# Performance work log

Measured on AMD Instinct MI355X. Metric: run time of the kernel, lower is better.

The kernel has to match this reference:

```python
import jax, jax.numpy as jnp
import numpy as np

EPS = 1e-5

def setup_inputs() -> dict:
    key = jax.random.key(0)
    ks = jax.random.split(key, 4)
    B, C, A, T = 32, 1536, 128, 1000  # batch, in_channels, attention_channels, time
    x = jax.random.normal(ks[0], (B, C, T), dtype=jnp.float32)
    # attention MLP: Conv1d(3C -> A, k=1) -> ReLU -> BN(A) -> Conv1d(A -> C, k=1)
    w1 = jax.random.normal(ks[1], (A, 3 * C), dtype=jnp.float32) / np.float32(np.sqrt(3 * C))
    b1 = jnp.zeros((A,), jnp.float32)
    g1 = jnp.ones((A,), jnp.float32)
    be1 = jnp.zeros((A,), jnp.float32)
    rm1 = jnp.zeros((A,), jnp.float32)
    rv1 = jnp.ones((A,), jnp.float32)
    w2 = jax.random.normal(ks[2], (C, A), dtype=jnp.float32) / np.float32(np.sqrt(A))
    b2 = jnp.zeros((C,), jnp.float32)
    # final BatchNorm1d over 2C pooled features
    g2 = jnp.ones((2 * C,), jnp.float32)
    be2 = jnp.zeros((2 * C,), jnp.float32)
    rm2 = jnp.zeros((2 * C,), jnp.float32)
    rv2 = jnp.ones((2 * C,), jnp.float32)
    return {"x": x, "w1": w1, "b1": b1, "g1": g1, "be1": be1, "rm1": rm1, "rv1": rv1,
            "w2": w2, "b2": b2, "g2": g2, "be2": be2, "rm2": rm2, "rv2": rv2}

def reference(x, w1, b1, g1, be1, rm1, rv1, w2, b2, g2, be2, rm2, rv2):
    # x: [B, C, T]
    mean_x = jnp.mean(x, axis=2, keepdims=True)                       # [B,C,1]
    std_x = jnp.sqrt(jnp.var(x, axis=2, ddof=1, keepdims=True) + EPS)  # unbiased var
    cat = jnp.concatenate([x,
                           jnp.broadcast_to(mean_x, x.shape),
                           jnp.broadcast_to(std_x, x.shape)], axis=1)  # [B,3C,T]
    # conv1x1 == channel matmul
    h = jnp.einsum('ac,bct->bat', w1, cat) + b1[None, :, None]         # [B,A,T]
    h = jax.nn.relu(h)
    # BatchNorm1d(A), inference mode with running stats
    h = (h - rm1[None, :, None]) * (g1 / jnp.sqrt(rv1 + EPS))[None, :, None] + be1[None, :, None]
    logits = jnp.einsum('ca,bat->bct', w2, h) + b2[None, :, None]      # [B,C,T]
    attn = jax.nn.softmax(logits, axis=2)
    xs = x * attn
    mu = jnp.sum(xs, axis=2)                                           # [B,C]
    sum_sq = jnp.sum(xs * x, axis=2)                                   # [B,C]
    sigma = jnp.sqrt(jnp.abs(sum_sq - mu ** 2) + EPS)
    pool = jnp.concatenate([mu, sigma], axis=1)                        # [B,2C]
    # final BatchNorm1d(2C), inference mode
    return (pool - rm2) * (g2 / jnp.sqrt(rv2 + EPS)) + be2
```

## Files before the change

### kernel.cpp

```cpp
#include <hip/hip_runtime.h>
#include <hip/hip_bf16.h>

#define BATCH 32
#define CCH   1536
#define ACH   128
#define TLEN  1000
#define TPAD  1024
#define NCB   (CCH / 64)
#define XTB   (TPAD * 64)
#define TSPLIT 4
#define TCHUNK 256
#define TSA   2
#define EPSV  1e-5f
#define NINF  -3.0e38f
#define LOG2E 1.4426950408889634f
#define RTHR  11.5f

typedef __attribute__((ext_vector_type(8))) short bf16x8;
typedef __attribute__((ext_vector_type(4))) float f32x4;

__device__ __forceinline__ unsigned short f2bf(float f) {
    union { float f; unsigned u; } v; v.f = f;
    unsigned r = v.u + 0x7fffu + ((v.u >> 16) & 1u);
    return (unsigned short)(r >> 16);
}
__device__ __forceinline__ float bf2f(unsigned short u) {
    union { unsigned u; float f; } v; v.u = ((unsigned)u) << 16;
    return v.f;
}

__global__ __launch_bounds__(512) void kA(const float* __restrict__ x,
                                          unsigned short* __restrict__ xt,
                                          float* __restrict__ st1,
                                          float* __restrict__ st2) {
    int b = blockIdx.y, cblk = blockIdx.x, ts = blockIdx.z;
    int cb = cblk * 64;
    int tbase = ts * (TPAD / TSA);
    int tid = threadIdx.x;
    int row = tid >> 3, l8 = tid & 7;
    __shared__ float tile[2][64][65];
    __shared__ float red1[8][64], red2[8][64];
    const float* xr = x + ((size_t)(b * CCH + cb + row)) * TLEN + tbase;
    unsigned short* xtp = xt + ((size_t)(b * NCB + cblk)) * XTB + (size_t)tbase * 64;

    float4 rA[2];
    float cs1[8], cs2[8];
    #pragma unroll
    for (int j = 0; j < 8; ++j) { cs1[j] = 0.f; cs2[j] = 0.f; }

    auto loadTile = [&](int it) {
        #pragma unroll
        for (int p = 0; p < 2; ++p) {
            int tf = it * 64 + p * 32 + l8 * 4;
            float4 vv = make_float4(0.f, 0.f, 0.f, 0.f);
            if (tbase + tf < TLEN) vv = *reinterpret_cast<const float4*>(xr + tf);
            rA[p] = vv;
        }
    };
    auto writeTile = [&](int buf) {
        #pragma unroll
        for (int p = 0; p < 2; ++p) {
            int tl = p * 32 + l8 * 4;
            tile[buf][tl + 0][row] = rA[p].x;
            tile[buf][tl + 1][row] = rA[p].y;
            tile[buf][tl + 2][row] = rA[p].z;
            tile[buf][tl + 3][row] = rA[p].w;
        }
    };
    auto readStore = [&](int buf, int it) {
        int tl = tid >> 3;
        int c8 = (tid & 7) * 8;
        float v[8];
        #pragma unroll
        for (int j = 0; j < 8; ++j) {
            v[j] = tile[buf][tl][c8 + j];
            cs1[j] += v[j];
            cs2[j] += v[j] * v[j];
        }
        unsigned o[4];
        #pragma unroll
        for (int j = 0; j < 4; ++j)
            o[j] = (unsigned)f2bf(v[2 * j]) | ((unsigned)f2bf(v[2 * j + 1]) << 16);
        uint4 u; u.x = o[0]; u.y = o[1]; u.z = o[2]; u.w = o[3];
        *reinterpret_cast<uint4*>(xtp + (size_t)(it * 64 + tl) * 64 + c8) = u;
    };

    const int NIT = (TPAD / TSA) / 64;
    loadTile(0);
    writeTile(0);
    loadTile(1);
    __syncthreads();
    for (int it = 0; it < NIT; ++it) {
        int buf = it & 1;
        if (it < NIT - 1) writeTile(buf ^ 1);
        if (it < NIT - 2) loadTile(it + 2);
        readStore(buf, it);
        __syncthreads();
    }

    #pragma unroll
    for (int j = 0; j < 8; ++j) {
        #pragma unroll
        for (int d = 8; d < 64; d <<= 1) {
            cs1[j] += __shfl_xor(cs1[j], d);
            cs2[j] += __shfl_xor(cs2[j], d);
        }
    }
    int wv = tid >> 6, lane = tid & 63;
    if (lane < 8) {
        #pragma unroll
        for (int j = 0; j < 8; ++j) {
            red1[wv][lane * 8 + j] = cs1[j];
            red2[wv][lane * 8 + j] = cs2[j];
        }
    }
    __syncthreads();
    if (tid < 64) {
        float s1 = 0.f, s2 = 0.f;
        #pragma unroll
        for (int w = 0; w < 8; ++w) { s1 += red1[w][tid]; s2 += red2[w][tid]; }
        st1[((size_t)ts * BATCH + b) * CCH + cb + tid] = s1;
        st2[((size_t)ts * BATCH + b) * CCH + cb + tid] = s2;
    }
}

__global__ __launch_bounds__(256) void kA2(const float* __restrict__ x,
                                           float* __restrict__ st1,
                                           float* __restrict__ st2) {
    int b = blockIdx.y, cb = blockIdx.x * 32;
    int tid = threadIdx.x;
    int row = tid >> 3, l8 = tid & 7;
    const float* xr = x + ((size_t)(b * CCH + cb + row)) * TLEN;
    float s1 = 0.f, s2 = 0.f;
    for (int tf = l8 * 4; tf < TLEN; tf += 32) {
        float4 vv = *reinterpret_cast<const float4*>(xr + tf);
        s1 += vv.x + vv.y + vv.z + vv.w;
        s2 += vv.x * vv.x + vv.y * vv.y + vv.z * vv.z + vv.w * vv.w;
    }
    #pragma unroll
    for (int d = 1; d < 8; d <<= 1) { s1 += __shfl_xor(s1, d); s2 += __shfl_xor(s2, d); }
    if (l8 == 0) {
        int idx = b * CCH + cb + row;
        st1[idx] = s1;
        st2[idx] = s2;
        st1[(size_t)BATCH * CCH + idx] = 0.f;
        st2[(size_t)BATCH * CCH + idx] = 0.f;
    }
}

__global__ __launch_bounds__(256) void kBW(const float* __restrict__ w1,
                                           unsigned short* __restrict__ w1x,
                                           const float* __restrict__ w2,
                                           const float* __restrict__ b2,
                                           const float* __restrict__ g1,
                                           const float* __restrict__ be1,
                                           const float* __restrict__ rm1,
                                           const float* __restrict__ rv1,
                                           unsigned short* __restrict__ w2e,
                                           float* __restrict__ b2e) {
    int bx = blockIdx.x;
    const int NB1 = (ACH * CCH) / 256;
    if (bx < NB1) {
        int e = bx * 256 + threadIdx.x;
        int a = e / CCH, c = e - a * CCH;
        w1x[e] = f2bf(w1[(size_t)a * (3 * CCH) + c]);
    } else {
        int c = (bx - NB1) * 4 + (threadIdx.x >> 6);
        int l = threadIdx.x & 63;
        float acc = 0.f;
        #pragma unroll
        for (int p = 0; p < 2; ++p) {
            int a = p * 64 + l;
            float s1 = g1[a] * rsqrtf(rv1[a] + EPSV);
            float w = w2[(size_t)c * ACH + a];
            w2e[(size_t)c * ACH + a] = f2bf(w * s1 * LOG2E);
            acc += w * (be1[a] - s1 * rm1[a]);
        }
        #pragma unroll
        for (int d = 1; d < 64; d <<= 1) acc += __shfl_xor(acc, d);
        if (l == 0) b2e[c] = (b2[c] + acc) * LOG2E;
    }
}

__global__ __launch_bounds__(64) void kB2n(const float* __restrict__ w1,
                                           const float* __restrict__ b1,
                                           const float* __restrict__ st1,
                                           const float* __restrict__ st2,
                                           float* __restrict__ hbias) {
    int a = blockIdx.x, b = blockIdx.y, l = threadIdx.x;
    const float* wr = w1 + (size_t)a * 3 * CCH;
    const float* p1 = st1 + (size_t)b * CCH;
    const float* p2 = st2 + (size_t)b * CCH;
    const size_t half = (size_t)BATCH * CCH;
    float acc = 0.f;
    const float invT = 1.f / (float)TLEN;
    const float invT1 = 1.f / (float)(TLEN - 1);
    for (int k = l; k < CCH; k += 64) {
        float s1 = p1[k] + p1[half + k];
        float s2 = p2[k] + p2[half + k];
        float mean = s1 * invT;
        float var = (s2 - s1 * s1 * invT) * invT1;
        float stdv = sqrtf(var + EPSV);
        acc += wr[CCH + k] * mean + wr[2 * CCH + k] * stdv;
    }
    #pragma unroll
    for (int d = 1; d < 64; d <<= 1) acc += __shfl_xor(acc, d);
    if (l == 0) hbias[b * ACH + a] = acc + b1[a];
}

__global__ __launch_bounds__(512) void kC3(const unsigned short* __restrict__ xt,
                                           const unsigned short* __restrict__ w1x,
                                           const float* __restrict__ hbias,
                                           unsigned short* __restrict__ h) {
    int b = blockIdx.y;
    int t0 = blockIdx.x * 64;
    int tid = threadIdx.x;
    int wv = tid >> 6, l = tid & 63, g = l >> 4, r = l & 15;
    int a0 = (wv & 3) * 32;
    int tw = (wv >> 2) * 32;

    __shared__ uint4 As[2][1024];
    __shared__ uint4 Bs[2][512];

    const unsigned short* bG = xt + (size_t)b * NCB * XTB;

    int qa0 = tid, qa1 = tid + 512, qb = tid;
    int wa0 = qa0 ^ ((qa0 >> 3) & 7), wa1 = qa1 ^ ((qa1 >> 3) & 7), wb = qb ^ ((qb >> 3) & 7);
    int arow0 = qa0 >> 3, arow1 = qa1 >> 3, acol = (qa0 & 7) * 8;
    int brow = qb >> 3, bcol = (qb & 7) * 8;

    As[0][wa0] = *reinterpret_cast<const uint4*>(w1x + (size_t)arow0 * CCH + acol);
    As[0][wa1] = *reinterpret_cast<const uint4*>(w1x + (size_t)arow1 * CCH + acol);
    Bs[0][wb]  = *reinterpret_cast<const uint4*>(bG + (size_t)(t0 + brow) * 64 + bcol);
    __syncthreads();

    f32x4 acc[2][2];
    #pragma unroll
    for (int i = 0; i < 2; ++i)
        #pragma unroll
        for (int j = 0; j < 2; ++j) acc[i][j] = f32x4{0.f, 0.f, 0.f, 0.f};

    for (int ks = 0; ks < CCH / 64; ++ks) {
        int buf = ks & 1;
        uint4 na0, na1, nb;
        if (ks < CCH / 64 - 1) {
            int cofs = (ks + 1) * 64;
            na0 = *reinterpret_cast<const uint4*>(w1x + (size_t)arow0 * CCH + cofs + acol);
            na1 = *reinterpret_cast<const uint4*>(w1x + (size_t)arow1 * CCH + cofs + acol);
            nb  = *reinterpret_cast<const uint4*>(bG + (size_t)(ks + 1) * XTB + (size_t)(t0 + brow) * 64 + bcol);
        }
        bf16x8 Af[2][2], Bf[2][2];
        #pragma unroll
        for (int at = 0; at < 2; ++at) {
            int row = a0 + 16 * at + r;
            #pragma unroll
            for (int kk = 0; kk < 2; ++kk) {
                int ch = (row * 8 + kk * 4 + g) ^ (row & 7);
                Af[at][kk] = *reinterpret_cast<const bf16x8*>(&As[buf][ch]);
            }
        }
        #pragma unroll
        for (int tt = 0; tt < 2; ++tt) {
            int row = tw + 16 * tt + r;
            #pragma unroll
            for (int kk = 0; kk < 2; ++kk) {
                int ch = (row * 8 + kk * 4 + g) ^ (row & 7);
                Bf[tt][kk] = *reinterpret_cast<const bf16x8*>(&Bs[buf][ch]);
            }
        }
        #pragma unroll
        for (int kk = 0; kk < 2; ++kk)
            #pragma unroll
            for (int at = 0; at < 2; ++at)
                #pragma unroll
                for (int tt = 0; tt < 2; ++tt)
                    acc[at][tt] = __builtin_amdgcn_mfma_f32_16x16x32_bf16(Af[at][kk], Bf[tt][kk], acc[at][tt], 0, 0, 0);
        if (ks < CCH / 64 - 1) {
            As[buf ^ 1][wa0] = na0;
            As[buf ^ 1][wa1] = na1;
            Bs[buf ^ 1][wb]  = nb;
        }
        __syncthreads();
    }

    #pragma unroll
    for (int at = 0; at < 2; ++at) {
        f32x4 hb = *reinterpret_cast<const f32x4*>(hbias + b * ACH + a0 + 16 * at + 4 * g);
        #pragma unroll
        for (int tt = 0; tt < 2; ++tt) {
            int t = t0 + tw + 16 * tt + r;
            float v0 = acc[at][tt][0] + hb[0]; v0 = v0 > 0.f ? v0 : 0.f;
            float v1 = acc[at][tt][1] + hb[1]; v1 = v1 > 0.f ? v1 : 0.f;
            float v2 = acc[at][tt][2] + hb[2]; v2 = v2 > 0.f ? v2 : 0.f;
            float v3 = acc[at][tt][3] + hb[3]; v3 = v3 > 0.f ? v3 : 0.f;
            uint2 u;
            u.x = (unsigned)f2bf(v0) | ((unsigned)f2bf(v1) << 16);
            u.y = (unsigned)f2bf(v2) | ((unsigned)f2bf(v3) << 16);
            *reinterpret_cast<uint2*>(h + ((size_t)(b * TPAD + t)) * ACH + a0 + 16 * at + 4 * g) = u;
        }
    }
}

__global__ __launch_bounds__(256) void kC2(const float* __restrict__ x,
                                           const unsigned short* __restrict__ w1x,
                                           const float* __restrict__ hbias,
                                           unsigned short* __restrict__ h) {
    int b = blockIdx.y;
    int t0 = blockIdx.x * 32;
    int tid = threadIdx.x;
    int wv = tid >> 6, l = tid & 63, g = l >> 4, r = l & 15;
    const unsigned short* aptr = w1x + (size_t)(32 * wv + r) * CCH + 8 * g;
    f32x4 acc[2][2];
    #pragma unroll
    for (int i = 0; i < 2; ++i)
        #pragma unroll
        for (int j = 0; j < 2; ++j) acc[i][j] = f32x4{0.f, 0.f, 0.f, 0.f};
    for (int kk = 0; kk < CCH / 32; ++kk) {
        bf16x8 Af[2], Bf[2];
        #pragma unroll
        for (int at = 0; at < 2; ++at)
            Af[at] = *reinterpret_cast<const bf16x8*>(aptr + (size_t)(16 * at) * CCH + 32 * kk);
        #pragma unroll
        for (int tt = 0; tt < 2; ++tt) {
            int t = t0 + 16 * tt + r;
            unsigned short tmp[8];
            #pragma unroll
            for (int j = 0; j < 8; ++j) {
                float xv = 0.f;
                if (t < TLEN) xv = x[((size_t)(b * CCH + 32 * kk + 8 * g + j)) * TLEN + t];
                tmp[j] = f2bf(xv);
            }
            Bf[tt] = *reinterpret_cast<const bf16x8*>(tmp);
        }
        #pragma unroll
        for (int at = 0; at < 2; ++at)
            #pragma unroll
            for (int tt = 0; tt < 2; ++tt)
                acc[at][tt] = __builtin_amdgcn_mfma_f32_16x16x32_bf16(Af[at], Bf[tt], acc[at][tt], 0, 0, 0);
    }
    #pragma unroll
    for (int at = 0; at < 2; ++at) {
        f32x4 hb = *reinterpret_cast<const f32x4*>(hbias + b * ACH + 32 * wv + 16 * at + 4 * g);
        #pragma unroll
        for (int tt = 0; tt < 2; ++tt) {
            int t = t0 + 16 * tt + r;
            float v0 = acc[at][tt][0] + hb[0]; v0 = v0 > 0.f ? v0 : 0.f;
            float v1 = acc[at][tt][1] + hb[1]; v1 = v1 > 0.f ? v1 : 0.f;
            float v2 = acc[at][tt][2] + hb[2]; v2 = v2 > 0.f ? v2 : 0.f;
            float v3 = acc[at][tt][3] + hb[3]; v3 = v3 > 0.f ? v3 : 0.f;
            uint2 u;
            u.x = (unsigned)f2bf(v0) | ((unsigned)f2bf(v1) << 16);
            u.y = (unsigned)f2bf(v2) | ((unsigned)f2bf(v3) << 16);
            *reinterpret_cast<uint2*>(h + ((size_t)(b * TPAD + t)) * ACH + 32 * wv + 16 * at + 4 * g) = u;
        }
    }
}

__global__ __launch_bounds__(256) void kD4(const unsigned short* __restrict__ xt,
                                           const unsigned short* __restrict__ h,
                                           const unsigned short* __restrict__ w2e,
                                           const float* __restrict__ b2e,
                                           float4* __restrict__ part) {
    int b = blockIdx.y, ts = blockIdx.z;
    int cblk = blockIdx.x * 128;
    int tid = threadIdx.x;
    int wv = tid >> 6, l = tid & 63, g = l >> 4, r = l & 15;
    int c0 = cblk + 32 * wv;
    int t0 = ts * TCHUNK;

    __shared__ uint4 hs[2][512];
    __shared__ uint2 xs[2][1024];

    bf16x8 W[2][4];
    f32x4 b2v[2];
    #pragma unroll
    for (int af = 0; af < 2; ++af) {
        #pragma unroll
        for (int kk = 0; kk < 4; ++kk)
            W[af][kk] = *reinterpret_cast<const bf16x8*>(w2e + (size_t)(c0 + 16 * af + r) * ACH + 32 * kk + 8 * g);
        b2v[af] = *reinterpret_cast<const f32x4*>(b2e + c0 + 16 * af + 4 * g);
    }

    const unsigned short* hbase = h + (size_t)(b * TPAD + t0) * ACH;
    const unsigned short* xpan = xt + ((size_t)b * NCB + (cblk >> 6)) * XTB;

    int q0 = tid, q1 = tid + 256;
    int w0 = q0 ^ ((q0 >> 4) & 7), w1 = q1 ^ ((q1 >> 4) & 7);
    int xtl = tid >> 3, xw7 = tid & 7;
    int xc0 = (xtl * 16 + xw7) ^ (xtl & 7);
    int xc1 = (xtl * 16 + 8 + xw7) ^ (xtl & 7);
    int xg[2];
    #pragma unroll
    for (int af = 0; af < 2; ++af) {
        int gx = 8 * wv + 4 * af + g;
        xg[af] = (r * 32 + gx) ^ ((r & 7) << 1);
    }

    auto ldH = [&](int tc, uint4& a, uint4& bq) {
        const unsigned short* src = hbase + (size_t)tc * 32 * ACH;
        a  = *reinterpret_cast<const uint4*>(src + q0 * 8);
        bq = *reinterpret_cast<const uint4*>(src + q1 * 8);
    };
    auto ldX = [&](int tc, uint4& a, uint4& bq) {
        size_t off = (size_t)(t0 + tc * 32 + xtl) * 64 + xw7 * 8;
        a  = *reinterpret_cast<const uint4*>(xpan + off);
        bq = *reinterpret_cast<const uint4*>(xpan + XTB + off);
    };

    {
        uint4 h0, h1, x0, x1;
        ldH(0, h0, h1); ldX(0, x0, x1);
        hs[0][w0] = h0; hs[0][w1] = h1;
        *reinterpret_cast<uint4*>(&xs[0][2 * xc0]) = x0;
        *reinterpret_cast<uint4*>(&xs[0][2 * xc1]) = x1;
    }
    __syncthreads();

    float m[2][4], s[2][4], wx[2][4], wxx[2][4];
    #pragma unroll
    for (int af = 0; af < 2; ++af)
        #pragma unroll
        for (int i = 0; i < 4; ++i) { m[af][i] = NINF; s[af][i] = 0.f; wx[af][i] = 0.f; wxx[af][i] = 0.f; }

    for (int tc = 0; tc < TCHUNK / 32; ++tc) {
        int buf = tc & 1;
        uint4 nh0, nh1, nx0, nx1;
        if (tc < TCHUNK / 32 - 1) {
            ldH(tc + 1, nh0, nh1);
            ldX(tc + 1, nx0, nx1);
        }

        f32x4 a2[2][2];
        a2[0][0] = f32x4{0.f, 0.f, 0.f, 0.f}; a2[0][1] = f32x4{0.f, 0.f, 0.f, 0.f};
        a2[1][0] = f32x4{0.f, 0.f, 0.f, 0.f}; a2[1][1] = f32x4{0.f, 0.f, 0.f, 0.f};
        #pragma unroll
        for (int tt = 0; tt < 2; ++tt) {
            int tl = tt * 16 + r;
            #pragma unroll
            for (int kk = 0; kk < 4; ++kk) {
                int ch = (tl * 16 + kk * 4 + g) ^ (tl & 7);
                bf16x8 Bf = *reinterpret_cast<const bf16x8*>(&hs[buf][ch]);
                a2[0][tt] = __builtin_amdgcn_mfma_f32_16x16x32_bf16(W[0][kk], Bf, a2[0][tt], 0, 0, 0);
                a2[1][tt] = __builtin_amdgcn_mfma_f32_16x16x32_bf16(W[1][kk], Bf, a2[1][tt], 0, 0, 0);
            }
        }

        int tb0 = t0 + tc * 32 + r, tb1 = tb0 + 16;
        bool val0 = (tb0 < TLEN), val1 = (tb1 < TLEN);
        #pragma unroll
        for (int af = 0; af < 2; ++af) {
            uint2 xu0 = xs[buf][xg[af]];
            uint2 xu1 = xs[buf][xg[af] + 512];
            float xv0[4], xv1[4];
            xv0[0] = bf2f((unsigned short)(xu0.x & 0xffff));
            xv0[1] = bf2f((unsigned short)(xu0.x >> 16));
            xv0[2] = bf2f((unsigned short)(xu0.y & 0xffff));
            xv0[3] = bf2f((unsigned short)(xu0.y >> 16));
            xv1[0] = bf2f((unsigned short)(xu1.x & 0xffff));
            xv1[1] = bf2f((unsigned short)(xu1.x >> 16));
            xv1[2] = bf2f((unsigned short)(xu1.y & 0xffff));
            xv1[3] = bf2f((unsigned short)(xu1.y >> 16));
            #pragma unroll
            for (int i = 0; i < 4; ++i) {
                float v0 = val0 ? (a2[af][0][i] + b2v[af][i]) : NINF;
                float v1 = val1 ? (a2[af][1][i] + b2v[af][i]) : NINF;
                float mx = fmaxf(v0, v1);
                if (__any(mx > m[af][i] + RTHR)) {
                    float mn = fmaxf(m[af][i], mx);
                    float sc = exp2f(m[af][i] - mn);
                    s[af][i] *= sc; wx[af][i] *= sc; wxx[af][i] *= sc; m[af][i] = mn;
                }
                float e0 = exp2f(v0 - m[af][i]);
                float e1 = exp2f(v1 - m[af][i]);
                float xe0 = xv0[i] * e0, xe1 = xv1[i] * e1;
                s[af][i]   += e0 + e1;
                wx[af][i]  += xe0 + xe1;
                wxx[af][i] += xv0[i] * xe0 + xv1[i] * xe1;
            }
        }

        if (tc < TCHUNK / 32 - 1) {
            hs[buf ^ 1][w0] = nh0;
            hs[buf ^ 1][w1] = nh1;
            *reinterpret_cast<uint4*>(&xs[buf ^ 1][2 * xc0]) = nx0;
            *reinterpret_cast<uint4*>(&xs[buf ^ 1][2 * xc1]) = nx1;
        }
        __syncthreads();
    }

    #pragma unroll
    for (int af = 0; af < 2; ++af)
        #pragma unroll
        for (int i = 0; i < 4; ++i) {
            float mm = m[af][i], ss = s[af][i], sx = wx[af][i], sxx = wxx[af][i];
            #pragma unroll
            for (int d = 1; d < 16; d <<= 1) {
                float mo = __shfl_xor(mm, d);
                float so = __shfl_xor(ss, d);
                float xo = __shfl_xor(sx, d);
                float qo = __shfl_xor(sxx, d);
                float mn = fmaxf(mm, mo);
                float fa = exp2f(mm - mn), fb = exp2f(mo - mn);
                ss = ss * fa + so * fb;
                sx = sx * fa + xo * fb;
                sxx = sxx * fa + qo * fb;
                mm = mn;
            }
            if (r == 0) {
                int c = c0 + 16 * af + 4 * g + i;
                float4 p; p.x = mm; p.y = ss; p.z = sx; p.w = sxx;
                part[((size_t)(b * TSPLIT + ts)) * CCH + c] = p;
            }
        }
}

__global__ __launch_bounds__(256) void kD1(const float* __restrict__ x,
                                           const unsigned short* __restrict__ h,
                                           const unsigned short* __restrict__ w2e,
                                           const float* __restrict__ b2e,
                                           float4* __restrict__ part) {
    int b = blockIdx.y, ts = blockIdx.z;
    int cblk = blockIdx.x * 64;
    int tid = threadIdx.x;
    int wv = tid >> 6, l = tid & 63, g = l >> 4, r = l & 15;
    int c0 = cblk + 16 * wv;
    int t0 = ts * TCHUNK;
    __shared__ float xsf[2][64][36];

    bf16x8 W[4];
    #pragma unroll
    for (int kk = 0; kk < 4; ++kk)
        W[kk] = *reinterpret_cast<const bf16x8*>(w2e + (size_t)(c0 + r) * ACH + 32 * kk + 8 * g);
    f32x4 b2v = *reinterpret_cast<const f32x4*>(b2e + c0 + 4 * g);

    int sc_ = tid >> 2;
    int st_ = (tid & 3) * 8;
    const float* xrow = x + ((size_t)(b * CCH + cblk + sc_)) * TLEN;
    const unsigned short* hb = h + (size_t)(b * TPAD) * ACH + 8 * g;

    auto stage = [&](int buf, int tc) {
        int tg = t0 + tc * 32;
        #pragma unroll
        for (int p = 0; p < 2; ++p) {
            int tl = st_ + 4 * p;
            float4 v = make_float4(0.f, 0.f, 0.f, 0.f);
            if (tg + tl < TLEN) v = *reinterpret_cast<const float4*>(xrow + tg + tl);
            *reinterpret_cast<float4*>(&xsf[buf][sc_][tl]) = v;
        }
    };

    float m[4], s[4], wx[4], wxx[4];
    #pragma unroll
    for (int i = 0; i < 4; ++i) { m[i] = NINF; s[i] = 0.f; wx[i] = 0.f; wxx[i] = 0.f; }

    stage(0, 0);
    __syncthreads();
    for (int tc = 0; tc < TCHUNK / 32; ++tc) {
        int buf = tc & 1;
        if (tc + 1 < TCHUNK / 32) stage(buf ^ 1, tc + 1);
        f32x4 a2[2];
        a2[0] = f32x4{0.f, 0.f, 0.f, 0.f};
        a2[1] = f32x4{0.f, 0.f, 0.f, 0.f};
        #pragma unroll
        for (int tt = 0; tt < 2; ++tt) {
            int t = t0 + tc * 32 + tt * 16 + r;
            #pragma unroll
            for (int kk = 0; kk < 4; ++kk) {
                bf16x8 Bf = *reinterpret_cast<const bf16x8*>(hb + (size_t)t * ACH + 32 * kk);
                a2[tt] = __builtin_amdgcn_mfma_f32_16x16x32_bf16(W[kk], Bf, a2[tt], 0, 0, 0);
            }
        }
        int tb = t0 + tc * 32 + r;
        bool val0 = (tb < TLEN), val1 = (tb + 16 < TLEN);
        #pragma unroll
        for (int i = 0; i < 4; ++i) {
            int cl = 16 * wv + 4 * g + i;
            float v0 = val0 ? (a2[0][i] + b2v[i]) : NINF;
            float v1 = val1 ? (a2[1][i] + b2v[i]) : NINF;
            float mx = fmaxf(v0, v1);
            if (mx > m[i] + RTHR) {
                float sc = exp2f(m[i] - mx);
                s[i] *= sc; wx[i] *= sc; wxx[i] *= sc; m[i] = mx;
            }
            float e0 = exp2f(v0 - m[i]);
            float e1 = exp2f(v1 - m[i]);
            float x0 = xsf[buf][cl][r];
            float x1 = xsf[buf][cl][r + 16];
            float xe0 = x0 * e0, xe1 = x1 * e1;
            s[i]   += e0 + e1;
            wx[i]  += xe0 + xe1;
            wxx[i] += x0 * xe0 + x1 * xe1;
        }
        __syncthreads();
    }

    #pragma unroll
    for (int i = 0; i < 4; ++i) {
        float mm = m[i], ss = s[i], sx = wx[i], sxx = wxx[i];
        #pragma unroll
        for (int d = 1; d < 16; d <<= 1) {
            float mo = __shfl_xor(mm, d);
            float so = __shfl_xor(ss, d);
            float xo = __shfl_xor(sx, d);
            float qo = __shfl_xor(sxx, d);
            float mn = fmaxf(mm, mo);
            float fa = exp2f(mm - mn), fb = exp2f(mo - mn);
            ss = ss * fa + so * fb;
            sx = sx * fa + xo * fb;
            sxx = sxx * fa + qo * fb;
            mm = mn;
        }
        if (r == 0) {
            int c = c0 + 4 * g + i;
            float4 p; p.x = mm; p.y = ss; p.z = sx; p.w = sxx;
            part[((size_t)(b * TSPLIT + ts)) * CCH + c] = p;
        }
    }
}

__global__ __launch_bounds__(256) void kE(const float4* __restrict__ part,
                                          const float* __restrict__ rm2,
                                          const float* __restrict__ rv2,
                                          const float* __restrict__ g2,
                                          const float* __restrict__ be2,
                                          float* __restrict__ out) {
    int idx = blockIdx.x * 256 + threadIdx.x;
    int b = idx / CCH, c = idx - b * CCH;
    float m = NINF, s = 0.f, wx = 0.f, wxx = 0.f;
    #pragma unroll
    for (int ts = 0; ts < TSPLIT; ++ts) {
        float4 p = part[((size_t)(b * TSPLIT + ts)) * CCH + c];
        float mn = fmaxf(m, p.x);
        float fa = exp2f(m - mn), fb = exp2f(p.x - mn);
        s = s * fa + p.y * fb;
        wx = wx * fa + p.z * fb;
        wxx = wxx * fa + p.w * fb;
        m = mn;
    }
    float mu = wx / s;
    float ssq = wxx / s;
    float sig = sqrtf(fabsf(ssq - mu * mu) + EPSV);
    out[b * 2 * CCH + c] = (mu - rm2[c]) * g2[c] * rsqrtf(rv2[c] + EPSV) + be2[c];
    int c2 = CCH + c;
    out[b * 2 * CCH + c2] = (sig - rm2[c2]) * g2[c2] * rsqrtf(rv2[c2] + EPSV) + be2[c2];
}

extern "C" void kernel_launch(void* const* d_in, const int* in_sizes, int n_in,
                              void* d_out, int out_size, void* d_ws, size_t ws_size,
                              hipStream_t stream) {
    const float* x   = (const float*)d_in[0];
    const float* w1  = (const float*)d_in[1];
    const float* b1  = (const float*)d_in[2];
    const float* g1  = (const float*)d_in[3];
    const float* be1 = (const float*)d_in[4];
    const float* rm1 = (const float*)d_in[5];
    const float* rv1 = (const float*)d_in[6];
    const float* w2  = (const float*)d_in[7];
    const float* b2  = (const float*)d_in[8];
    const float* g2  = (const float*)d_in[9];
    const float* be2 = (const float*)d_in[10];
    const float* rm2 = (const float*)d_in[11];
    const float* rv2 = (const float*)d_in[12];
    float* out = (float*)d_out;

    const size_t sz_xt    = (size_t)BATCH * NCB * XTB * 2;
    const size_t sz_h     = (size_t)BATCH * TPAD * ACH * 2;
    const size_t sz_w1x   = (size_t)ACH * CCH * 2;
    const size_t sz_w2e   = (size_t)CCH * ACH * 2;
    const size_t sz_st    = (size_t)TSA * BATCH * CCH * 4;
    const size_t sz_hbias = (size_t)BATCH * ACH * 4;
    const size_t sz_b2e   = (size_t)CCH * 4;
    const size_t sz_part  = (size_t)BATCH * TSPLIT * CCH * 16;
    const size_t need_small = sz_h + sz_w1x + sz_w2e + 2 * sz_st
                            + sz_hbias + sz_b2e + sz_part;
    bool use_xt = (ws_size >= need_small + sz_xt);

    char* ws = (char*)d_ws;
    unsigned short* xt = nullptr;
    if (use_xt) { xt = (unsigned short*)ws; ws += sz_xt; }
    unsigned short* hbuf = (unsigned short*)ws; ws += sz_h;
    unsigned short* w1x  = (unsigned short*)ws; ws += sz_w1x;
    unsigned short* w2e  = (unsigned short*)ws; ws += sz_w2e;
    float* st1   = (float*)ws; ws += sz_st;
    float* st2   = (float*)ws; ws += sz_st;
    float* hbias = (float*)ws; ws += sz_hbias;
    float* b2e   = (float*)ws; ws += sz_b2e;
    float4* part = (float4*)ws; ws += sz_part;

    const int NBW = (ACH * CCH) / 256 + CCH / 4;
    if (use_xt)
        kA<<<dim3(NCB, BATCH, TSA), 512, 0, stream>>>(x, xt, st1, st2);
    else
        kA2<<<dim3(48, 32), 256, 0, stream>>>(x, st1, st2);
    kBW<<<NBW, 256, 0, stream>>>(w1, w1x, w2, b2, g1, be1, rm1, rv1, w2e, b2e);
    kB2n<<<dim3(ACH, BATCH), 64, 0, stream>>>(w1, b1, st1, st2, hbias);
    if (use_xt) {
        kC3<<<dim3(TPAD / 64, BATCH), 512, 0, stream>>>(xt, w1x, hbias, hbuf);
        kD4<<<dim3(CCH / 128, BATCH, TSPLIT), 256, 0, stream>>>(xt, hbuf, w2e, b2e, part);
    } else {
        kC2<<<dim3(TPAD / 32, BATCH), 256, 0, stream>>>(x, w1x, hbias, hbuf);
        kD1<<<dim3(CCH / 64, BATCH, TSPLIT), 256, 0, stream>>>(x, hbuf, w2e, b2e, part);
    }
    kE<<<(BATCH * CCH) / 256, 256, 0, stream>>>(part, rm2, rv2, g2, be2, out);
}
```

Baseline: 143.7 us.

## Fuse first and second attention matmuls with softmax pooling into one kernel

The kernel that computed the hidden activation h now keeps its 64-timestep tile of h in shared memory and immediately runs the second matmul, softmax partials and weighted moments over all channels, writing per-chunk partials. This removes the global write and re-read of h and one kernel launch. In exchange there are 16 time chunks per batch instead of 4, so the partial buffer and the final combine grow. Each block also loops over all 1536 channels with an extra pair of block barriers per step, which could lengthen the critical path.

Result: slower. 195.0 us (+35.7%).

```diff
diff --git a/kernel.cpp b/kernel.cpp
--- a/kernel.cpp
+++ b/kernel.cpp
@@ -8,6 +8,7 @@
 #define TPAD  1024
 #define NCB   (CCH / 64)
 #define XTB   (TPAD * 64)
+#define NCHK  16
 #define TSPLIT 4
 #define TCHUNK 256
 #define TSA   2
@@ -208,10 +209,12 @@
     if (l == 0) hbias[b * ACH + a] = acc + b1[a];
 }
 
-__global__ __launch_bounds__(512) void kC3(const unsigned short* __restrict__ xt,
+__global__ __launch_bounds__(512) void kCD(const unsigned short* __restrict__ xt,
                                            const unsigned short* __restrict__ w1x,
                                            const float* __restrict__ hbias,
-                                           unsigned short* __restrict__ h) {
+                                           const unsigned short* __restrict__ w2e,
+                                           const float* __restrict__ b2e,
+                                           float4* __restrict__ part) {
     int b = blockIdx.y;
     int t0 = blockIdx.x * 64;
     int tid = threadIdx.x;
@@ -221,6 +224,8 @@
 
     __shared__ uint4 As[2][1024];
     __shared__ uint4 Bs[2][512];
+    __shared__ uint2 hsl[2048];
+    __shared__ uint2 xs[2048];
 
     const unsigned short* bG = xt + (size_t)b * NCB * XTB;
 
@@ -283,20 +288,113 @@
         __syncthreads();
     }
 
-    #pragma unroll
-    for (int at = 0; at < 2; ++at) {
-        f32x4 hb = *reinterpret_cast<const f32x4*>(hbias + b * ACH + a0 + 16 * at + 4 * g);
-        #pragma unroll
-        for (int tt = 0; tt < 2; ++tt) {
-            int t = t0 + tw + 16 * tt + r;
-            float v0 = acc[at][tt][0] + hb[0]; v0 = v0 > 0.f ? v0 : 0.f;
-            float v1 = acc[at][tt][1] + hb[1]; v1 = v1 > 0.f ? v1 : 0.f;
-            float v2 = acc[at][tt][2] + hb[2]; v2 = v2 > 0.f ? v2 : 0.f;
-            float v3 = acc[at][tt][3] + hb[3]; v3 = v3 > 0.f ? v3 : 0.f;
-            uint2 u;
-            u.x = (unsigned)f2bf(v0) | ((unsigned)f2bf(v1) << 16);
-            u.y = (unsigned)f2bf(v2) | ((unsigned)f2bf(v3) << 16);
-            *reinterpret_cast<uint2*>(h + ((size_t)(b * TPAD + t)) * ACH + a0 + 16 * at + 4 * g) = u;
+    int xtl_ = tid >> 3, xcw = tid & 7;
+    auto xsrc = [&](int s, int p) {
+        return reinterpret_cast<const uint4*>(bG + (size_t)(2 * s + p) * XTB
+                                              + (size_t)(t0 + xtl_) * 64 + xcw * 8);
+    };
+    uint4 px0 = *xsrc(0, 0);
+    uint4 px1 = *xsrc(0, 1);
+
+    {
+        f32x4 hb0 = *reinterpret_cast<const f32x4*>(hbias + b * ACH + a0 + 4 * g);
+        f32x4 hb1 = *reinterpret_cast<const f32x4*>(hbias + b * ACH + a0 + 16 + 4 * g);
+        #pragma unroll
+        for (int at = 0; at < 2; ++at) {
+            f32x4 hb = at ? hb1 : hb0;
+            #pragma unroll
+            for (int tt = 0; tt < 2; ++tt) {
+                int t = tw + 16 * tt + r;
+                float v0 = acc[at][tt][0] + hb[0]; v0 = v0 > 0.f ? v0 : 0.f;
+                float v1 = acc[at][tt][1] + hb[1]; v1 = v1 > 0.f ? v1 : 0.f;
+                float v2 = acc[at][tt][2] + hb[2]; v2 = v2 > 0.f ? v2 : 0.f;
+                float v3 = acc[at][tt][3] + hb[3]; v3 = v3 > 0.f ? v3 : 0.f;
+                uint2 u;
+                u.x = (unsigned)f2bf(v0) | ((unsigned)f2bf(v1) << 16);
+                u.y = (unsigned)f2bf(v2) | ((unsigned)f2bf(v3) << 16);
+                int ccol = 4 * (wv & 3) + 2 * at + (g >> 1);
+                int ch = (t * 16 + ccol) ^ (t & 7);
+                hsl[ch * 2 + (g & 1)] = u;
+            }
+        }
+        int g0 = ((xtl_ * 32 + 2 * xcw) ^ ((xtl_ & 7) << 1));
+        int g1i = ((xtl_ * 32 + 16 + 2 * xcw) ^ ((xtl_ & 7) << 1));
+        *reinterpret_cast<uint4*>(&xs[g0]) = px0;
+        *reinterpret_cast<uint4*>(&xs[g1i]) = px1;
+    }
+    __syncthreads();
+
+    for (int s = 0; s < CCH / 128; ++s) {
+        uint4 nx0, nx1;
+        if (s < CCH / 128 - 1) {
+            nx0 = *xsrc(s + 1, 0);
+            nx1 = *xsrc(s + 1, 1);
+        }
+        int c0s = s * 128;
+        int crow = c0s + 16 * wv + r;
+        bf16x8 Wf[4];
+        #pragma unroll
+        for (int kk = 0; kk < 4; ++kk)
+            Wf[kk] = *reinterpret_cast<const bf16x8*>(w2e + (size_t)crow * ACH + 32 * kk + 8 * g);
+        f32x4 acc2[4];
+        #pragma unroll
+        for (int tt = 0; tt < 4; ++tt) acc2[tt] = f32x4{0.f, 0.f, 0.f, 0.f};
+        #pragma unroll
+        for (int tt = 0; tt < 4; ++tt) {
+            int t = 16 * tt + r;
+            #pragma unroll
+            for (int kk = 0; kk < 4; ++kk) {
+                int ch = (t * 16 + kk * 4 + g) ^ (t & 7);
+                bf16x8 Hf = *reinterpret_cast<const bf16x8*>(&hsl[ch * 2]);
+                acc2[tt] = __builtin_amdgcn_mfma_f32_16x16x32_bf16(Wf[kk], Hf, acc2[tt], 0, 0, 0);
+            }
+        }
+        f32x4 b2v = *reinterpret_cast<const f32x4*>(b2e + c0s + 16 * wv + 4 * g);
+        uint2 xu[4];
+        #pragma unroll
+        for (int tt = 0; tt < 4; ++tt)
+            xu[tt] = xs[(((16 * tt + r) << 5) | (4 * wv + g)) ^ ((r & 7) << 1)];
+
+        #pragma unroll
+        for (int i = 0; i < 4; ++i) {
+            float v[4];
+            #pragma unroll
+            for (int tt = 0; tt < 4; ++tt) {
+                int t = t0 + 16 * tt + r;
+                v[tt] = (t < TLEN) ? (acc2[tt][i] + b2v[i]) : NINF;
+            }
+            float mm = fmaxf(fmaxf(v[0], v[1]), fmaxf(v[2], v[3]));
+            #pragma unroll
+            for (int d = 1; d < 16; d <<= 1) mm = fmaxf(mm, __shfl_xor(mm, d));
+            float ss = 0.f, sx = 0.f, sxx = 0.f;
+            #pragma unroll
+            for (int tt = 0; tt < 4; ++tt) {
+                float e = exp2f(v[tt] - mm);
+                unsigned w = (i & 2) ? xu[tt].y : xu[tt].x;
+                float xv = bf2f((unsigned short)((i & 1) ? (w >> 16) : (w & 0xffff)));
+                float xe = xv * e;
+                ss += e; sx += xe; sxx += xv * xe;
+            }
+            #pragma unroll
+            for (int d = 1; d < 16; d <<= 1) {
+                ss += __shfl_xor(ss, d);
+                sx += __shfl_xor(sx, d);
+                sxx += __shfl_xor(sxx, d);
+            }
+            if (r == 0) {
+                int c = c0s + 16 * wv + 4 * g + i;
+                float4 p; p.x = mm; p.y = ss; p.z = sx; p.w = sxx;
+                part[((size_t)(b * NCHK + blockIdx.x)) * CCH + c] = p;
+            }
+        }
+
+        if (s < CCH / 128 - 1) {
+            __syncthreads();
+            int g0 = ((xtl_ * 32 + 2 * xcw) ^ ((xtl_ & 7) << 1));
+            int g1i = ((xtl_ * 32 + 16 + 2 * xcw) ^ ((xtl_ & 7) << 1));
+            *reinterpret_cast<uint4*>(&xs[g0]) = nx0;
+            *reinterpret_cast<uint4*>(&xs[g1i]) = nx1;
+            __syncthreads();
         }
     }
 }
@@ -354,164 +452,6 @@
             *reinterpret_cast<uint2*>(h + ((size_t)(b * TPAD + t)) * ACH + 32 * wv + 16 * at + 4 * g) = u;
         }
     }
-}
-
-__global__ __launch_bounds__(256) void kD4(const unsigned short* __restrict__ xt,
-                                           const unsigned short* __restrict__ h,
-                                           const unsigned short* __restrict__ w2e,
-                                           const float* __restrict__ b2e,
-                                           float4* __restrict__ part) {
-    int b = blockIdx.y, ts = blockIdx.z;
-    int cblk = blockIdx.x * 128;
-    int tid = threadIdx.x;
-    int wv = tid >> 6, l = tid & 63, g = l >> 4, r = l & 15;
-    int c0 = cblk + 32 * wv;
-    int t0 = ts * TCHUNK;
-
-    __shared__ uint4 hs[2][512];
-    __shared__ uint2 xs[2][1024];
-
-    bf16x8 W[2][4];
-    f32x4 b2v[2];
-    #pragma unroll
-    for (int af = 0; af < 2; ++af) {
-        #pragma unroll
-        for (int kk = 0; kk < 4; ++kk)
-            W[af][kk] = *reinterpret_cast<const bf16x8*>(w2e + (size_t)(c0 + 16 * af + r) * ACH + 32 * kk + 8 * g);
-        b2v[af] = *reinterpret_cast<const f32x4*>(b2e + c0 + 16 * af + 4 * g);
-    }
-
-    const unsigned short* hbase = h + (size_t)(b * TPAD + t0) * ACH;
-    const unsigned short* xpan = xt + ((size_t)b * NCB + (cblk >> 6)) * XTB;
-
-    int q0 = tid, q1 = tid + 256;
-    int w0 = q0 ^ ((q0 >> 4) & 7), w1 = q1 ^ ((q1 >> 4) & 7);
-    int xtl = tid >> 3, xw7 = tid & 7;
-    int xc0 = (xtl * 16 + xw7) ^ (xtl & 7);
-    int xc1 = (xtl * 16 + 8 + xw7) ^ (xtl & 7);
-    int xg[2];
-    #pragma unroll
-    for (int af = 0; af < 2; ++af) {
-        int gx = 8 * wv + 4 * af + g;
-        xg[af] = (r * 32 + gx) ^ ((r & 7) << 1);
-    }
-
-    auto ldH = [&](int tc, uint4& a, uint4& bq) {
-        const unsigned short* src = hbase + (size_t)tc * 32 * ACH;
-        a  = *reinterpret_cast<const uint4*>(src + q0 * 8);
-        bq = *reinterpret_cast<const uint4*>(src + q1 * 8);
-    };
-    auto ldX = [&](int tc, uint4& a, uint4& bq) {
-        size_t off = (size_t)(t0 + tc * 32 + xtl) * 64 + xw7 * 8;
-        a  = *reinterpret_cast<const uint4*>(xpan + off);
-        bq = *reinterpret_cast<const uint4*>(xpan + XTB + off);
-    };
-
-    {
-        uint4 h0, h1, x0, x1;
-        ldH(0, h0, h1); ldX(0, x0, x1);
-        hs[0][w0] = h0; hs[0][w1] = h1;
-        *reinterpret_cast<uint4*>(&xs[0][2 * xc0]) = x0;
-        *reinterpret_cast<uint4*>(&xs[0][2 * xc1]) = x1;
-    }
-    __syncthreads();
-
-    float m[2][4], s[2][4], wx[2][4], wxx[2][4];
-    #pragma unroll
-    for (int af = 0; af < 2; ++af)
-        #pragma unroll
-        for (int i = 0; i < 4; ++i) { m[af][i] = NINF; s[af][i] = 0.f; wx[af][i] = 0.f; wxx[af][i] = 0.f; }
-
-    for (int tc = 0; tc < TCHUNK / 32; ++tc) {
-        int buf = tc & 1;
-        uint4 nh0, nh1, nx0, nx1;
-        if (tc < TCHUNK / 32 - 1) {
-            ldH(tc + 1, nh0, nh1);
-            ldX(tc + 1, nx0, nx1);
-        }
-
-        f32x4 a2[2][2];
-        a2[0][0] = f32x4{0.f, 0.f, 0.f, 0.f}; a2[0][1] = f32x4{0.f, 0.f, 0.f, 0.f};
-        a2[1][0] = f32x4{0.f, 0.f, 0.f, 0.f}; a2[1][1] = f32x4{0.f, 0.f, 0.f, 0.f};
-        #pragma unroll
-        for (int tt = 0; tt < 2; ++tt) {
-            int tl = tt * 16 + r;
-            #pragma unroll
-            for (int kk = 0; kk < 4; ++kk) {
-                int ch = (tl * 16 + kk * 4 + g) ^ (tl & 7);
-                bf16x8 Bf = *reinterpret_cast<const bf16x8*>(&hs[buf][ch]);
-                a2[0][tt] = __builtin_amdgcn_mfma_f32_16x16x32_bf16(W[0][kk], Bf, a2[0][tt], 0, 0, 0);
-                a2[1][tt] = __builtin_amdgcn_mfma_f32_16x16x32_bf16(W[1][kk], Bf, a2[1][tt], 0, 0, 0);
-            }
-        }
-
-        int tb0 = t0 + tc * 32 + r, tb1 = tb0 + 16;
-        bool val0 = (tb0 < TLEN), val1 = (tb1 < TLEN);
-        #pragma unroll
-        for (int af = 0; af < 2; ++af) {
-            uint2 xu0 = xs[buf][xg[af]];
-            uint2 xu1 = xs[buf][xg[af] + 512];
-            float xv0[4], xv1[4];
-            xv0[0] = bf2f((unsigned short)(xu0.x & 0xffff));
-            xv0[1] = bf2f((unsigned short)(xu0.x >> 16));
-            xv0[2] = bf2f((unsigned short)(xu0.y & 0xffff));
-            xv0[3] = bf2f((unsigned short)(xu0.y >> 16));
-            xv1[0] = bf2f((unsigned short)(xu1.x & 0xffff));
-            xv1[1] = bf2f((unsigned short)(xu1.x >> 16));
-            xv1[2] = bf2f((unsigned short)(xu1.y & 0xffff));
-            xv1[3] = bf2f((unsigned short)(xu1.y >> 16));
-            #pragma unroll
-            for (int i = 0; i < 4; ++i) {
-                float v0 = val0 ? (a2[af][0][i] + b2v[af][i]) : NINF;
-                float v1 = val1 ? (a2[af][1][i] + b2v[af][i]) : NINF;
-                float mx = fmaxf(v0, v1);
-                if (__any(mx > m[af][i] + RTHR)) {
-                    float mn = fmaxf(m[af][i], mx);
-                    float sc = exp2f(m[af][i] - mn);
-                    s[af][i] *= sc; wx[af][i] *= sc; wxx[af][i] *= sc; m[af][i] = mn;
-                }
-                float e0 = exp2f(v0 - m[af][i]);
-                float e1 = exp2f(v1 - m[af][i]);
-                float xe0 = xv0[i] * e0, xe1 = xv1[i] * e1;
-                s[af][i]   += e0 + e1;
-                wx[af][i]  += xe0 + xe1;
-                wxx[af][i] += xv0[i] * xe0 + xv1[i] * xe1;
-            }
-        }
-
-        if (tc < TCHUNK / 32 - 1) {
-            hs[buf ^ 1][w0] = nh0;
-            hs[buf ^ 1][w1] = nh1;
-            *reinterpret_cast<uint4*>(&xs[buf ^ 1][2 * xc0]) = nx0;
-            *reinterpret_cast<uint4*>(&xs[buf ^ 1][2 * xc1]) = nx1;
-        }
-        __syncthreads();
-    }
-
-    #pragma unroll
-    for (int af = 0; af < 2; ++af)
-        #pragma unroll
-        for (int i = 0; i < 4; ++i) {
-            float mm = m[af][i], ss = s[af][i], sx = wx[af][i], sxx = wxx[af][i];
-            #pragma unroll
-            for (int d = 1; d < 16; d <<= 1) {
-                float mo = __shfl_xor(mm, d);
-                float so = __shfl_xor(ss, d);
-                float xo = __shfl_xor(sx, d);
-                float qo = __shfl_xor(sxx, d);
-                float mn = fmaxf(mm, mo);
-                float fa = exp2f(mm - mn), fb = exp2f(mo - mn);
-                ss = ss * fa + so * fb;
-                sx = sx * fa + xo * fb;
-                sxx = sxx * fa + qo * fb;
-                mm = mn;
-            }
-            if (r == 0) {
-                int c = c0 + 16 * af + 4 * g + i;
-                float4 p; p.x = mm; p.y = ss; p.z = sx; p.w = sxx;
-                part[((size_t)(b * TSPLIT + ts)) * CCH + c] = p;
-            }
-        }
 }
 
 __global__ __launch_bounds__(256) void kD1(const float* __restrict__ x,
@@ -619,6 +559,7 @@
 }
 
 __global__ __launch_bounds__(256) void kE(const float4* __restrict__ part,
+                                          int nchk,
                                           const float* __restrict__ rm2,
                                           const float* __restrict__ rv2,
                                           const float* __restrict__ g2,
@@ -627,9 +568,8 @@
     int idx = blockIdx.x * 256 + threadIdx.x;
     int b = idx / CCH, c = idx - b * CCH;
     float m = NINF, s = 0.f, wx = 0.f, wxx = 0.f;
-    #pragma unroll
-    for (int ts = 0; ts < TSPLIT; ++ts) {
-        float4 p = part[((size_t)(b * TSPLIT + ts)) * CCH + c];
+    for (int ts = 0; ts < nchk; ++ts) {
+        float4 p = part[((size_t)(b * nchk + ts)) * CCH + c];
         float mn = fmaxf(m, p.x);
         float fa = exp2f(m - mn), fb = exp2f(p.x - mn);
         s = s * fa + p.y * fb;
@@ -670,7 +610,7 @@
     const size_t sz_st    = (size_t)TSA * BATCH * CCH * 4;
     const size_t sz_hbias = (size_t)BATCH * ACH * 4;
     const size_t sz_b2e   = (size_t)CCH * 4;
-    const size_t sz_part  = (size_t)BATCH * TSPLIT * CCH * 16;
+    const size_t sz_part  = (size_t)BATCH * NCHK * CCH * 16;
     const size_t need_small = sz_h + sz_w1x + sz_w2e + 2 * sz_st
                             + sz_hbias + sz_b2e + sz_part;
     bool use_xt = (ws_size >= need_small + sz_xt);
@@ -695,11 +635,11 @@
     kBW<<<NBW, 256, 0, stream>>>(w1, w1x, w2, b2, g1, be1, rm1, rv1, w2e, b2e);
     kB2n<<<dim3(ACH, BATCH), 64, 0, stream>>>(w1, b1, st1, st2, hbias);
     if (use_xt) {
-        kC3<<<dim3(TPAD / 64, BATCH), 512, 0, stream>>>(xt, w1x, hbias, hbuf);
-        kD4<<<dim3(CCH / 128, BATCH, TSPLIT), 256, 0, stream>>>(xt, hbuf, w2e, b2e, part);
+        kCD<<<dim3(TPAD / 64, BATCH), 512, 0, stream>>>(xt, w1x, hbias, w2e, b2e, part);
+        kE<<<(BATCH * CCH) / 256, 256, 0, stream>>>(part, NCHK, rm2, rv2, g2, be2, out);
     } else {
         kC2<<<dim3(TPAD / 32, BATCH), 256, 0, stream>>>(x, w1x, hbias, hbuf);
         kD1<<<dim3(CCH / 64, BATCH, TSPLIT), 256, 0, stream>>>(x, hbuf, w2e, b2e, part);
-    }
-    kE<<<(BATCH * CCH) / 256, 256, 0, stream>>>(part, rm2, rv2, g2, be2, out);
-}
+        kE<<<(BATCH * CCH) / 256, 256, 0, stream>>>(part, TSPLIT, rm2, rv2, g2, be2, out);
+    }
+}
```
